# Kernel tuning notes

Hardware: AMD Instinct MI355X
Metric: run time of the kernel (lower is better)

The kernel has to match this reference:

```python
import jax, jax.numpy as jnp
import numpy as np
from jax.scipy.linalg import solve_triangular

B, L, HID, NH = 2, 1024, 1024, 4
DK = DV = 256
CONV_K, CHUNK, FIR_S_K, FIR_L_K = 4, 32, 3, 31
GATE_IN = HID + 3 * DV * 4 + DV * 4  # 5120
GATE_H = 2 * DV  # 512


def _l2norm(x):
    return x * jax.lax.rsqrt(jnp.sum(x * x, -1, keepdims=True) + 1e-6)


def _short_conv(x, w):
    # causal depthwise conv1d + silu. x: [b,l,c], w: [c,k]
    c, k = w.shape
    y = jax.lax.conv_general_dilated(x.transpose(0, 2, 1), w[:, None, :], (1,),
                                     [(k - 1, 0)], feature_group_count=c)
    return jax.nn.silu(y.transpose(0, 2, 1))


def _fir(x, f):
    # per-head depthwise causal FIR. x: [b,l,h,d], f: [h,d,k]
    b, l, h, d = x.shape
    k = f.shape[-1]
    xf = x.transpose(0, 2, 3, 1).reshape(b, h * d, l)
    y = jax.lax.conv_general_dilated(xf, f.reshape(h * d, 1, k), (1,),
                                     [(k - 1, 0)], feature_group_count=h * d)
    return y.reshape(b, h, d, l).transpose(0, 3, 1, 2)


def _delta_rule(q, k, v, beta, chunk=CHUNK):
    # q,k: [b,h,L,dk], v: [b,h,L,dv], beta: [b,h,L]; L % chunk == 0
    b, h, l, dk = q.shape
    dv = v.shape[-1]
    n = l // chunk
    q = _l2norm(q)
    k = _l2norm(k)
    v = v * beta[..., None]
    kb = k * beta[..., None]
    rs = lambda t: t.reshape(b, h, n, chunk, -1)
    q, k, v, kb = map(rs, (q, k, v, kb))
    # UT transform: serial forward substitution == unit-lower triangular solve
    A = -jnp.tril(jnp.einsum('bhncd,bhned->bhnce', kb, k), -1)  # strictly lower
    eye = jnp.eye(chunk, dtype=q.dtype)
    T = solve_triangular(eye - A, jnp.broadcast_to(eye, A.shape), lower=True)
    u = T @ v   # [b,h,n,c,dv]
    w = T @ kb  # [b,h,n,c,dk]
    mov = lambda t: jnp.moveaxis(t, 2, 0)

    def step(S, inp):
        qi, ki, ui, wi = inp  # [b,h,c,d]
        attn = jnp.tril(qi @ ki.transpose(0, 1, 3, 2))  # causal incl. diag
        u_i = ui - wi @ S
        o_i = qi @ S + attn @ u_i
        return S + ki.transpose(0, 1, 3, 2) @ u_i, o_i

    S0 = jnp.zeros((b, h, dk, dv), dtype=q.dtype)
    S, o = jax.lax.scan(step, S0, (mov(q), mov(k), mov(u), mov(w)))
    o = jnp.moveaxis(o, 0, 2).reshape(b, h, l, dv)
    return o, S


def _gate(hidden, branches, W1, b1, W2, b2, temp, eps_floor):
    def stats(p):
        m = p.mean(-1, keepdims=True)
        r = jnp.sqrt(jnp.clip((p * p).mean(-1, keepdims=True), 1e-8))
        mx = p.max(-1, keepdims=True)
        return jnp.concatenate([jnp.broadcast_to(m, p.shape),
                                jnp.broadcast_to(r, p.shape),
                                jnp.broadcast_to(mx, p.shape)], -1)

    b, l, h, d = branches[0].shape
    hb = jnp.broadcast_to(hidden[:, :, None, :], (b, l, h, hidden.shape[-1]))
    head_in = jnp.concatenate([hb] + [stats(p) for p in branches] + list(branches), -1)
    hmid = jax.nn.gelu(head_in @ W1 + b1, approximate=False)
    logits = hmid @ W2 + b2  # [b,l,h,4]
    t = jnp.clip(temp, 0.2, 10.0)[None, None, :, None]
    w = jax.nn.softmax(logits / t, -1)
    floor = jnp.clip(eps_floor, 1e-7, 0.1)[None, None]
    w = jnp.maximum(w, floor)
    return w / w.sum(-1, keepdims=True)


def setup_inputs() -> dict:
    key = jax.random.key(0)
    ks = jax.random.split(key, 16)
    s = 0.02
    inp = {
        'x': jax.random.normal(ks[0], (B, L, HID), jnp.float32),
        'Wq': jax.random.normal(ks[1], (HID, NH * DK), jnp.float32) * s,
        'Wk': jax.random.normal(ks[2], (HID, NH * DK), jnp.float32) * s,
        'Wv': jax.random.normal(ks[3], (HID, NH * DV), jnp.float32) * s,
        'Wb': jax.random.normal(ks[4], (HID, NH), jnp.float32) * s,
        'qc_w': jax.random.normal(ks[5], (NH * DK, CONV_K), jnp.float32) * 0.5,
        'kc_w': jax.random.normal(ks[6], (NH * DK, CONV_K), jnp.float32) * 0.5,
        'vc_w': jax.random.normal(ks[7], (NH * DV, CONV_K), jnp.float32) * 0.5,
        'gW1': jax.random.normal(ks[10], (GATE_IN, GATE_H), jnp.float32) * s,
        'gb1': jnp.zeros((GATE_H,), jnp.float32),
        'gW2': jax.random.normal(ks[11], (GATE_H, 4), jnp.float32) * s,
        'gb2': jnp.zeros((4,), jnp.float32),
        'temp': jnp.ones((NH,), jnp.float32),
        'eps_floor': jnp.full((NH, 4), 0.01, jnp.float32),
        'onorm_w': jnp.ones((DV,), jnp.float32),
        'Wo': jax.random.normal(ks[12], (NH * DV, HID), jnp.float32) * s,
    }
    # FIR filters: identity tap at last position + small noise (matches init intent)
    fs = jnp.zeros((NH, DV, FIR_S_K)).at[..., -1].set(1.0)
    fl = jnp.zeros((NH, DV, FIR_L_K)).at[..., -1].set(1.0)
    inp['fir_s'] = fs + s * jax.random.normal(ks[8], fs.shape, jnp.float32)
    inp['fir_l'] = fl + s * jax.random.normal(ks[9], fl.shape, jnp.float32)
    return inp


def reference(x, Wq, Wk, Wv, Wb, qc_w, kc_w, vc_w, fir_s, fir_l,
              gW1, gb1, gW2, gb2, temp, eps_floor, onorm_w, Wo):
    b, l, _ = x.shape
    q = _short_conv(x @ Wq, qc_w).reshape(b, l, NH, DK)
    k = _short_conv(x @ Wk, kc_w).reshape(b, l, NH, DK)
    v = _short_conv(x @ Wv, vc_w).reshape(b, l, NH, DV)
    beta = jax.nn.sigmoid(x @ Wb)  # [b,l,h]
    tr = lambda t: t.transpose(0, 2, 1, 3)
    delta_o, _ = _delta_rule(tr(q), tr(k), tr(v), beta.transpose(0, 2, 1))
    delta_o = tr(delta_o)  # [b,l,h,dv]
    branches = [_fir(v, fir_s), _fir(v, fir_l), delta_o, v]
    w = _gate(x, branches, gW1, gb1, gW2, gb2, temp, eps_floor)
    o = sum(w[..., i:i + 1] * branches[i] for i in range(4))
    o = o * jax.lax.rsqrt((o * o).mean(-1, keepdims=True) + 1e-5) * onorm_w
    return o.reshape(b, l, NH * DV) @ Wo
```

## Files before the change

### kernel.cpp

```cpp
#include <hip/hip_runtime.h>
#include <math.h>

#define BB 2
#define LL 1024
#define HIDD 1024
#define NH 4
#define DD 256
#define NCH 32
#define ROWS 2048
#define HROWS 8192

typedef long long i64;
typedef unsigned short u16t;
typedef unsigned int u32t;
typedef __attribute__((ext_vector_type(8))) short short8;
typedef __attribute__((ext_vector_type(4))) float f32x4;
#define MFMA_BF16(a, b, c) __builtin_amdgcn_mfma_f32_16x16x32_bf16(a, b, c, 0, 0, 0)

__device__ __forceinline__ float sigmoidf_(float x) { return 1.0f / (1.0f + expf(-x)); }

__device__ __forceinline__ u16t f2bf(float f) {
  u32t u = __float_as_uint(f);
  u = u + 0x7FFFu + ((u >> 16) & 1u);
  return (u16t)(u >> 16);
}
__device__ __forceinline__ u32t pk2(u16t a, u16t b) { return (u32t)a | ((u32t)b << 16); }

__device__ __forceinline__ u32t cvt_pk_bf16(float lo, float hi) {
  u32t r;
  asm("v_cvt_pk_bf16_f32 %0, %1, %2" : "=v"(r) : "v"(lo), "v"(hi));
  return r;
}

__device__ __forceinline__ void async_load16(const u16t* g, u16t* l) {
  __builtin_amdgcn_global_load_lds(
      (const __attribute__((address_space(1))) u32t*)g,
      (__attribute__((address_space(3))) u32t*)l, 16, 0, 0);
}

__device__ __forceinline__ void barrier_lds_only() {
  asm volatile("s_waitcnt lgkmcnt(0)" ::: "memory");
  __builtin_amdgcn_s_barrier();
  asm volatile("" ::: "memory");
}

template<int N>
__device__ __forceinline__ void block_reduce_sum(float* v, float* scratch) {
  int lane = threadIdx.x & 63, wid = threadIdx.x >> 6;
#pragma unroll
  for (int i = 0; i < N; i++) {
    float x = v[i];
#pragma unroll
    for (int off = 1; off < 64; off <<= 1) x += __shfl_xor(x, off);
    if (lane == 0) scratch[wid * N + i] = x;
  }
  __syncthreads();
#pragma unroll
  for (int i = 0; i < N; i++)
    v[i] = scratch[i] + scratch[N + i] + scratch[2 * N + i] + scratch[3 * N + i];
  __syncthreads();
}

__device__ __forceinline__ void transcast_body(
    const float* __restrict__ in, int ldin, u16t* __restrict__ out, int ldout,
    int nbi, int kbi, float (*tile)[33]) {
  int tx = threadIdx.x & 31, ty = threadIdx.x >> 5;
  int nb = nbi * 32, kb = kbi * 32;
#pragma unroll
  for (int r = 0; r < 4; r++)
    tile[ty + r * 8][tx] = in[(i64)(kb + ty + r * 8) * ldin + nb + tx];
  __syncthreads();
#pragma unroll
  for (int r = 0; r < 4; r++)
    out[(i64)(nb + ty + r * 8) * ldout + kb + tx] = f2bf(tile[tx][ty + r * 8]);
}

__global__ __launch_bounds__(256) void prep_kernel(
    const float* __restrict__ Wq, const float* __restrict__ Wk, const float* __restrict__ Wv,
    const float* __restrict__ x, const float* __restrict__ Wb,
    u16t* __restrict__ WqkvT, u16t* __restrict__ xbf, float* __restrict__ betab) {
  __shared__ float tile[32][33];
  int blk = blockIdx.x, t = threadIdx.x;
  if (blk < 3072) {
    int m = blk >> 10, bi = blk & 1023;
    const float* in = m == 0 ? Wq : m == 1 ? Wk : Wv;
    transcast_body(in, 1024, WqkvT + (i64)m * 1024 * 1024, 1024, bi & 31, bi >> 5, tile);
  } else if (blk < 5120) {
    i64 e = ((i64)(blk - 3072) * 256 + t) * 4;
    float4 v = *(const float4*)(x + e);
    uint2 o;
    o.x = pk2(f2bf(v.x), f2bf(v.y));
    o.y = pk2(f2bf(v.z), f2bf(v.w));
    *(uint2*)(xbf + e) = o;
  } else {
    int row = blk - 5120;
    float a[4] = {0, 0, 0, 0};
    for (int c = t; c < 1024; c += 256) {
      float xv = x[(i64)row * 1024 + c];
      float4 wv = *(const float4*)(Wb + c * 4);
      a[0] += xv * wv.x; a[1] += xv * wv.y; a[2] += xv * wv.z; a[3] += xv * wv.w;
    }
    block_reduce_sum<4>(a, (float*)tile);
    if (t == 0) {
#pragma unroll
      for (int g = 0; g < 4; g++) betab[row * 4 + g] = sigmoidf_(a[g]);
    }
  }
}

__device__ __forceinline__ void gemm_bt_body(
    const u16t* __restrict__ A, const u16t* __restrict__ B,
    float* __restrict__ C, int K, int ldc, int n0, int m0,
    u16t* As, u16t* Bs) {
  int t = threadIdx.x;
  int w = t >> 6, lane = t & 63;
  int l15 = lane & 15, quad = lane >> 4;
  int wm = (w & 1) * 64, wn = (w >> 1) * 64;
  f32x4 acc[4][4] = {};
  int c0 = 2 * w, c1 = 2 * w + 1;
  int srow0 = c0 * 16 + (lane >> 2);
  int srow1 = c1 * 16 + (lane >> 2);
  int scol = (lane & 3) * 8;
  const u16t* Ag0 = A + (i64)(m0 + srow0) * K + scol;
  const u16t* Ag1 = A + (i64)(m0 + srow1) * K + scol;
  const u16t* Bg0 = B + (i64)(n0 + srow0) * K + scol;
  const u16t* Bg1 = B + (i64)(n0 + srow1) * K + scol;
  u16t* As0 = As + c0 * 512;
  u16t* As1 = As + c1 * 512;
  u16t* Bs0 = Bs + c0 * 512;
  u16t* Bs1 = Bs + c1 * 512;
  for (int k0 = 0; k0 < K; k0 += 32) {
    async_load16(Ag0 + k0, As0);
    async_load16(Ag1 + k0, As1);
    async_load16(Bg0 + k0, Bs0);
    async_load16(Bg1 + k0, Bs1);
    __syncthreads();
    short8 a[4], b[4];
#pragma unroll
    for (int mt = 0; mt < 4; mt++)
      a[mt] = *(const short8*)&As[(wm + mt * 16 + l15) * 32 + quad * 8];
#pragma unroll
    for (int nt = 0; nt < 4; nt++)
      b[nt] = *(const short8*)&Bs[(wn + nt * 16 + l15) * 32 + quad * 8];
#pragma unroll
    for (int mt = 0; mt < 4; mt++)
#pragma unroll
      for (int nt = 0; nt < 4; nt++)
        acc[mt][nt] = MFMA_BF16(a[mt], b[nt], acc[mt][nt]);
    __syncthreads();
  }
#pragma unroll
  for (int mt = 0; mt < 4; mt++) {
    int r0 = m0 + wm + mt * 16 + quad * 4;
#pragma unroll
    for (int nt = 0; nt < 4; nt++) {
      int cc = n0 + wn + nt * 16 + l15;
#pragma unroll
      for (int rg = 0; rg < 4; rg++)
        C[(i64)(r0 + rg) * ldc + cc] = acc[mt][nt][rg];
    }
  }
}

__global__ __launch_bounds__(256) void gemm_bt_kernel(
    const u16t* __restrict__ A, const u16t* __restrict__ B,
    float* __restrict__ C, int K, int ldc) {
  __shared__ u16t As[128 * 32];
  __shared__ u16t Bs[128 * 32];
  gemm_bt_body(A, B, C, K, ldc, blockIdx.x * 128, blockIdx.y * 128, As, Bs);
}

__global__ __launch_bounds__(256) void conv_silu3_kernel(
    const float* __restrict__ pre, const float* __restrict__ qw,
    const float* __restrict__ kw, const float* __restrict__ vw,
    float* __restrict__ qo, float* __restrict__ ko, float* __restrict__ vo,
    u16t* __restrict__ brcat) {
  int seg = blockIdx.x >> 11;
  int row = blockIdx.x & 2047;
  int l = row & 1023;
  int c = threadIdx.x * 4;
  const float* w = seg == 0 ? qw : seg == 1 ? kw : vw;
  float* out = seg == 0 ? qo : seg == 1 ? ko : vo;
  float4 w0 = *(const float4*)(w + (i64)(c + 0) * 4);
  float4 w1 = *(const float4*)(w + (i64)(c + 1) * 4);
  float4 w2 = *(const float4*)(w + (i64)(c + 2) * 4);
  float4 w3 = *(const float4*)(w + (i64)(c + 3) * 4);
  const float* base = pre + (i64)row * 3072 + (seg << 10) + c;
  float4 x0 = *(const float4*)(base);
  float4 acc;
  acc.x = w0.w * x0.x; acc.y = w1.w * x0.y; acc.z = w2.w * x0.z; acc.w = w3.w * x0.w;
  if (l >= 1) {
    float4 xm = *(const float4*)(base - 3072);
    acc.x += w0.z * xm.x; acc.y += w1.z * xm.y; acc.z += w2.z * xm.z; acc.w += w3.z * xm.w;
  }
  if (l >= 2) {
    float4 xm = *(const float4*)(base - 2 * 3072);
    acc.x += w0.y * xm.x; acc.y += w1.y * xm.y; acc.z += w2.y * xm.z; acc.w += w3.y * xm.w;
  }
  if (l >= 3) {
    float4 xm = *(const float4*)(base - 3 * 3072);
    acc.x += w0.x * xm.x; acc.y += w1.x * xm.y; acc.z += w2.x * xm.z; acc.w += w3.x * xm.w;
  }
  float4 r;
  r.x = acc.x * sigmoidf_(acc.x);
  r.y = acc.y * sigmoidf_(acc.y);
  r.z = acc.z * sigmoidf_(acc.z);
  r.w = acc.w * sigmoidf_(acc.w);
  *(float4*)(out + (i64)row * 1024 + c) = r;
  if (seg == 2) {
    uint2 o;
    o.x = cvt_pk_bf16(r.x, r.y);
    o.y = cvt_pk_bf16(r.z, r.w);
    *(uint2*)(brcat + ((i64)row * 4 + (c >> 8)) * 1024 + 768 + (c & 255)) = o;
  }
}

__global__ __launch_bounds__(256) void preprocess_kernel(
    const float* __restrict__ q, const float* __restrict__ k, const float* __restrict__ v,
    const float* __restrict__ beta, float* __restrict__ qn, float* __restrict__ kn,
    float* __restrict__ vb, float* __restrict__ kb, u16t* __restrict__ qnbf) {
  int t = threadIdx.x, lane = t & 63, wv = t >> 6;
  int row = blockIdx.x * 4 + wv;
  i64 base = (i64)row * 256 + lane * 4;
  float4 q4 = *(const float4*)(q + base);
  float4 k4 = *(const float4*)(k + base);
  float4 v4 = *(const float4*)(v + base);
  float s2[2];
  s2[0] = q4.x * q4.x + q4.y * q4.y + q4.z * q4.z + q4.w * q4.w;
  s2[1] = k4.x * k4.x + k4.y * k4.y + k4.z * k4.z + k4.w * k4.w;
#pragma unroll
  for (int off = 1; off < 64; off <<= 1) {
    s2[0] += __shfl_xor(s2[0], off);
    s2[1] += __shfl_xor(s2[1], off);
  }
  float qi = rsqrtf(s2[0] + 1e-6f), ki = rsqrtf(s2[1] + 1e-6f);
  float bet = beta[row];
  float4 qn4, kn4, vb4, kb4;
  qn4.x = q4.x * qi; qn4.y = q4.y * qi; qn4.z = q4.z * qi; qn4.w = q4.w * qi;
  kn4.x = k4.x * ki; kn4.y = k4.y * ki; kn4.z = k4.z * ki; kn4.w = k4.w * ki;
  vb4.x = v4.x * bet; vb4.y = v4.y * bet; vb4.z = v4.z * bet; vb4.w = v4.w * bet;
  kb4.x = kn4.x * bet; kb4.y = kn4.y * bet; kb4.z = kn4.z * bet; kb4.w = kn4.w * bet;
  *(float4*)(qn + base) = qn4;
  *(float4*)(kn + base) = kn4;
  *(float4*)(vb + base) = vb4;
  *(float4*)(kb + base) = kb4;
  int b = row >> 12, l = (row >> 2) & 1023, h = row & 3;
  uint2 o;
  o.x = cvt_pk_bf16(qn4.x, qn4.y);
  o.y = cvt_pk_bf16(qn4.z, qn4.w);
  *(uint2*)(qnbf + ((i64)(b * 4 + h) * 1024 + l) * 256 + lane * 4) = o;
}

__global__ __launch_bounds__(256) void phaseA2_kernel(
    const float* __restrict__ qn, const float* __restrict__ kn,
    const float* __restrict__ vb, const float* __restrict__ kb,
    float* __restrict__ u_g, u16t* __restrict__ w_bf, u16t* __restrict__ attn_bf,
    u16t* __restrict__ knT,
    const float* __restrict__ gW1, const float* __restrict__ Wo,
    u16t* __restrict__ W1hT, u16t* __restrict__ W1bT, u16t* __restrict__ WoT,
    float* __restrict__ wsum) {
  __shared__ __attribute__((aligned(16))) char smem[37376];
  int blk = blockIdx.x, t = threadIdx.x;
  if (blk < 256) {
    float (*KN)[260] = (float(*)[260])smem;
    float (*Ms)[32] = (float(*)[32])(smem + 33280);
    int i = blk & 31, bh = blk >> 5;
    int rbase = ((bh >> 2) * LL + i * 32) * NH + (bh & 3);
    i64 bhn = blk;
#pragma unroll
    for (int ii = 0; ii < 8; ii++) {
      int fid = t + ii * 256;
      int c = fid >> 6, dq = (fid & 63) << 2;
      *(float4*)&KN[c][dq] = *(const float4*)(kn + (i64)(rbase + c * NH) * 256 + dq);
    }
    __syncthreads();
    int c = t >> 3, e0 = (t & 7) * 4;
    const float* kbp = kb + (i64)(rbase + c * NH) * 256;
    const float* qp = qn + (i64)(rbase + c * NH) * 256;
    float am[4] = {0, 0, 0, 0}, aa[4] = {0, 0, 0, 0};
    for (int d = 0; d < 256; d += 4) {
      float4 kv = *(const float4*)(kbp + d);
      float4 qv = *(const float4*)(qp + d);
#pragma unroll
      for (int z = 0; z < 4; z++) {
        float4 nv = *(const float4*)&KN[e0 + z][d];
        am[z] += kv.x * nv.x + kv.y * nv.y + kv.z * nv.z + kv.w * nv.w;
        aa[z] += qv.x * nv.x + qv.y * nv.y + qv.z * nv.z + qv.w * nv.w;
      }
    }
    {
      uint2 o;
      u16t a0 = (e0 + 0 <= c) ? f2bf(aa[0]) : 0;
      u16t a1 = (e0 + 1 <= c) ? f2bf(aa[1]) : 0;
      u16t a2 = (e0 + 2 <= c) ? f2bf(aa[2]) : 0;
      u16t a3 = (e0 + 3 <= c) ? f2bf(aa[3]) : 0;
      o.x = pk2(a0, a1); o.y = pk2(a2, a3);
      *(uint2*)(attn_bf + bhn * 1024 + c * 32 + e0) = o;
    }
#pragma unroll
    for (int z = 0; z < 4; z++) {
      int e = e0 + z;
      Ms[c][e] = (e < c) ? am[z] : 0.0f;
    }
    __syncthreads();
    float uc[32], wc[32];
#pragma unroll
    for (int cc = 0; cc < 32; cc++) {
      float uval = vb[(i64)(rbase + cc * NH) * 256 + t];
      float wval = kb[(i64)(rbase + cc * NH) * 256 + t];
#pragma unroll
      for (int c2 = 0; c2 < cc; c2++) {
        float m = Ms[cc][c2];
        uval -= m * uc[c2];
        wval -= m * wc[c2];
      }
      uc[cc] = uval; wc[cc] = wval;
      u_g[(bhn * 32 + cc) * 256 + t] = uval;
      w_bf[(bhn * 32 + cc) * 256 + t] = f2bf(-wval);
    }
    int d = t;
    u16t o[32];
#pragma unroll
    for (int cc = 0; cc < 32; cc++) o[cc] = f2bf(KN[cc][d]);
#pragma unroll
    for (int z = 0; z < 4; z++) {
      uint4 vv;
      vv.x = pk2(o[z * 8 + 0], o[z * 8 + 1]);
      vv.y = pk2(o[z * 8 + 2], o[z * 8 + 3]);
      vv.z = pk2(o[z * 8 + 4], o[z * 8 + 5]);
      vv.w = pk2(o[z * 8 + 6], o[z * 8 + 7]);
      *(uint4*)(knT + (bhn * 256 + d) * 32 + z * 8) = vv;
    }
  } else if (blk < 2304) {
    float (*tile)[33] = (float(*)[33])smem;
    int pb = blk - 256;
    if (pb < 1024) {
      int which = pb >> 9, bi = pb & 511;
      const float* in = gW1 + (which ? (i64)4096 * 512 : 0);
      transcast_body(in, 512, which ? W1bT : W1hT, 1024, bi & 15, bi >> 4, tile);
    } else {
      int bi = pb - 1024;
      transcast_body(Wo, 1024, WoT, 1024, bi & 31, bi >> 5, tile);
    }
  } else {
    int bi = blk - 2304;
    int s12 = bi >> 1, col = (bi & 1) * 256 + t;
    const float* p = gW1 + (i64)(1024 + s12 * 256) * 512 + col;
    float acc = 0.0f;
    for (int r = 0; r < 256; r++) acc += p[(i64)r * 512];
    wsum[s12 * 512 + col] = acc;
  }
}

#define SROW 264
struct ScanBuf {
  short8 m8[8];
  f32x4 uc4;
  short8 af;
  short8 kf[4];
};

__device__ void delta_scan_body(
    int blk,
    const u16t* __restrict__ wbf, const u16t* __restrict__ knT,
    const float* __restrict__ u_g, const u16t* __restrict__ qnbf,
    const u16t* __restrict__ attnbf,
    float* __restrict__ dlt, u16t* __restrict__ brcat,
    u16t* Sbf, u16t* Ubf) {
  int t = threadIdx.x, w = t >> 6, lane = t & 63;
  int l15 = lane & 15, quad = lane >> 4;
  int bh = blk & 7, jb = blk >> 3, j0 = jb * 16;
  int b_ = bh >> 2, h_ = bh & 3;
  bool isU = (w < 2);
  int wc = isU ? w : (w - 2);
  for (int idx = t; idx < 16 * SROW; idx += 256) Sbf[idx] = 0;
  f32x4 accS[4] = {};
  __syncthreads();
  __builtin_amdgcn_s_setprio(1);

  auto load_chunk = [&](int i, ScanBuf& B) {
    i64 bhn = (i64)bh * 32 + i;
    const u16t* mbase = isU
        ? wbf + (bhn * 32 + wc * 16 + l15) * 256 + quad * 8
        : qnbf + ((i64)bh * 1024 + i * 32 + wc * 16 + l15) * 256 + quad * 8;
#pragma unroll
    for (int kd = 0; kd < 8; kd++) B.m8[kd] = *(const short8*)(mbase + kd * 32);
    if (isU) {
      int cm = wc * 16 + quad * 4;
#pragma unroll
      for (int r = 0; r < 4; r++)
        B.uc4[r] = u_g[(bhn * 32 + cm + r) * 256 + j0 + l15];
    } else {
      B.af = *(const short8*)(attnbf + bhn * 1024 + (wc * 16 + l15) * 32 + quad * 8);
    }
#pragma unroll
    for (int dt = 0; dt < 4; dt++)
      B.kf[dt] = *(const short8*)(knT + (bhn * 256 + w * 64 + dt * 16 + l15) * 32 + quad * 8);
  };

  auto process = [&](int i, ScanBuf& B) {
    f32x4 zero = {};
    f32x4 ca = isU ? B.uc4 : zero;
    f32x4 cb = zero;
#pragma unroll
    for (int kd = 0; kd < 4; kd++) {
      short8 sfa = *(const short8*)&Sbf[l15 * SROW + kd * 32 + quad * 8];
      short8 sfb = *(const short8*)&Sbf[l15 * SROW + (kd + 4) * 32 + quad * 8];
      ca = MFMA_BF16(B.m8[kd], sfa, ca);
      cb = MFMA_BF16(B.m8[kd + 4], sfb, cb);
    }
    f32x4 cacc;
#pragma unroll
    for (int r = 0; r < 4; r++) cacc[r] = ca[r] + cb[r];
    if (isU) {
      int cm = wc * 16 + quad * 4;
      uint2 o;
      o.x = cvt_pk_bf16(cacc[0], cacc[1]);
      o.y = cvt_pk_bf16(cacc[2], cacc[3]);
      *(uint2*)&Ubf[l15 * 40 + cm] = o;
    }
    barrier_lds_only();
    short8 bu = *(const short8*)&Ubf[l15 * 40 + quad * 8];
    if (!isU) {
      cacc = MFMA_BF16(B.af, bu, cacc);
#pragma unroll
      for (int rg = 0; rg < 4; rg++) {
        int l = i * 32 + wc * 16 + quad * 4 + rg;
        i64 row = ((i64)b_ * 1024 + l) * 4 + h_;
        dlt[row * 256 + j0 + l15] = cacc[rg];
        brcat[row * 1024 + 512 + j0 + l15] = f2bf(cacc[rg]);
      }
    }
#pragma unroll
    for (int dt = 0; dt < 4; dt++) accS[dt] = MFMA_BF16(B.kf[dt], bu, accS[dt]);
#pragma unroll
    for (int dt = 0; dt < 4; dt++) {
      uint2 o;
      o.x = cvt_pk_bf16(accS[dt][0], accS[dt][1]);
      o.y = cvt_pk_bf16(accS[dt][2], accS[dt][3]);
      *(uint2*)&Sbf[l15 * SROW + w * 64 + dt * 16 + quad * 4] = o;
    }
    barrier_lds_only();
  };

  ScanBuf b0, b1;
  load_chunk(0, b0);
#pragma unroll 1
  for (int ii = 0; ii < 16; ii++) {
    int i = ii * 2;
    load_chunk(i + 1, b1);
    process(i, b0);
    if (ii < 15) load_chunk(i + 2, b0);
    process(i + 1, b1);
  }
  __builtin_amdgcn_s_setprio(0);
}

__device__ void fir2_body(
    int blk, const float* __restrict__ v,
    const float* __restrict__ f_s, const float* __restrict__ f_l,
    float* __restrict__ fs, float* __restrict__ fl, u16t* __restrict__ brcat) {
  int t = threadIdx.x;
  int b = blk >> 8, h = (blk >> 6) & 3, lc = blk & 63;
  int l0 = lc * 16;
  float flw[31], fsw[3];
  const float* flp = f_l + ((i64)h * 256 + t) * 31;
#pragma unroll
  for (int j = 0; j < 31; j++) flw[j] = flp[j];
  const float* fsp = f_s + ((i64)h * 256 + t) * 3;
#pragma unroll
  for (int j = 0; j < 3; j++) fsw[j] = fsp[j];
  float win[46];
#pragma unroll
  for (int r = 0; r < 46; r++) {
    int l = l0 - 30 + r;
    win[r] = (l >= 0) ? v[(((i64)b * 1024 + l) * 4 + h) * 256 + t] : 0.0f;
  }
#pragma unroll
  for (int i = 0; i < 16; i++) {
    float al = 0.0f;
#pragma unroll
    for (int j = 0; j < 31; j++) al += flw[j] * win[i + j];
    float as = fsw[0] * win[i + 28] + fsw[1] * win[i + 29] + fsw[2] * win[i + 30];
    i64 row = ((i64)b * 1024 + (l0 + i)) * 4 + h;
    fs[row * 256 + t] = as;
    fl[row * 256 + t] = al;
    brcat[row * 1024 + t] = f2bf(as);
    brcat[row * 1024 + 256 + t] = f2bf(al);
  }
}

__global__ __launch_bounds__(256) void mega5_kernel(
    const u16t* __restrict__ wbf, const u16t* __restrict__ knT,
    const float* __restrict__ u_g, const u16t* __restrict__ qnbf,
    const u16t* __restrict__ attnbf, float* __restrict__ dlt, u16t* __restrict__ brcat,
    const float* __restrict__ vbuf, const float* __restrict__ firs,
    const float* __restrict__ firl, float* __restrict__ fs, float* __restrict__ fl,
    const u16t* __restrict__ xbf, const u16t* __restrict__ W1hT,
    float* __restrict__ hbase) {
  __shared__ __attribute__((aligned(16))) char smem[16384];
  int blk = blockIdx.x;
  if (blk < 128) {
    u16t* Sbf = (u16t*)smem;
    u16t* Ubf = Sbf + 16 * SROW;
    delta_scan_body(blk, wbf, knT, u_g, qnbf, attnbf, dlt, brcat, Sbf, Ubf);
  } else if (blk < 640) {
    fir2_body(blk - 128, vbuf, firs, firl, fs, fl, brcat);
  } else {
    int bi = blk - 640;
    u16t* As = (u16t*)smem;
    u16t* Bs = As + 128 * 32;
    gemm_bt_body(xbf, W1hT, hbase, 1024, 512, (bi & 3) * 128, (bi >> 2) * 128, As, Bs);
  }
}

__global__ __launch_bounds__(256) void gatemix_kernel(
    const float* __restrict__ hbase, const float* __restrict__ brW,
    const float* __restrict__ wsum,
    const float* __restrict__ gb1, const float* __restrict__ gW2,
    const float* __restrict__ gb2, const float* __restrict__ temp,
    const float* __restrict__ epsf,
    const float* __restrict__ fs, const float* __restrict__ fl,
    const float* __restrict__ dlt, const float* __restrict__ v,
    const float* __restrict__ onw, u16t* __restrict__ out) {
  int t = threadIdx.x, lane = t & 63, wv = t >> 6;
  int row = blockIdx.x * 4 + wv;
  int bl = row >> 2, h = row & 3;
  i64 base = (i64)row * 256 + lane * 4;
  float4 vfs = *(const float4*)(fs + base);
  float4 vfl = *(const float4*)(fl + base);
  float4 vdl = *(const float4*)(dlt + base);
  float4 vvv = *(const float4*)(v + base);
  float r8[8];
  r8[0] = vfs.x + vfs.y + vfs.z + vfs.w;
  r8[1] = vfs.x * vfs.x + vfs.y * vfs.y + vfs.z * vfs.z + vfs.w * vfs.w;
  r8[2] = vfl.x + vfl.y + vfl.z + vfl.w;
  r8[3] = vfl.x * vfl.x + vfl.y * vfl.y + vfl.z * vfl.z + vfl.w * vfl.w;
  r8[4] = vdl.x + vdl.y + vdl.z + vdl.w;
  r8[5] = vdl.x * vdl.x + vdl.y * vdl.y + vdl.z * vdl.z + vdl.w * vdl.w;
  r8[6] = vvv.x + vvv.y + vvv.z + vvv.w;
  r8[7] = vvv.x * vvv.x + vvv.y * vvv.y + vvv.z * vvv.z + vvv.w * vvv.w;
#pragma unroll
  for (int off = 1; off < 64; off <<= 1) {
#pragma unroll
    for (int i = 0; i < 8; i++) r8[i] += __shfl_xor(r8[i], off);
  }
  float m4[4];
  m4[0] = fmaxf(fmaxf(vfs.x, vfs.y), fmaxf(vfs.z, vfs.w));
  m4[1] = fmaxf(fmaxf(vfl.x, vfl.y), fmaxf(vfl.z, vfl.w));
  m4[2] = fmaxf(fmaxf(vdl.x, vdl.y), fmaxf(vdl.z, vdl.w));
  m4[3] = fmaxf(fmaxf(vvv.x, vvv.y), fmaxf(vvv.z, vvv.w));
#pragma unroll
  for (int off = 1; off < 64; off <<= 1) {
#pragma unroll
    for (int i = 0; i < 4; i++) m4[i] = fmaxf(m4[i], __shfl_xor(m4[i], off));
  }
  float st[12];
#pragma unroll
  for (int p = 0; p < 4; p++) {
    st[p * 3 + 0] = r8[p * 2] * (1.0f / 256.0f);
    st[p * 3 + 1] = sqrtf(fmaxf(r8[p * 2 + 1] * (1.0f / 256.0f), 1e-8f));
    st[p * 3 + 2] = m4[p];
  }
  float lg[4] = {0, 0, 0, 0};
#pragma unroll
  for (int jj = 0; jj < 8; jj++) {
    int o = jj * 64 + lane;
    float hm = hbase[(i64)bl * 512 + o] + brW[(i64)row * 512 + o] + gb1[o];
#pragma unroll
    for (int s = 0; s < 12; s++) hm += st[s] * wsum[s * 512 + o];
    float ge = 0.5f * hm * (1.0f + erff(hm * 0.70710678118654752f));
    float4 w2 = *(const float4*)(gW2 + o * 4);
    lg[0] += ge * w2.x; lg[1] += ge * w2.y; lg[2] += ge * w2.z; lg[3] += ge * w2.w;
  }
#pragma unroll
  for (int off = 1; off < 64; off <<= 1) {
#pragma unroll
    for (int i = 0; i < 4; i++) lg[i] += __shfl_xor(lg[i], off);
  }
  float tt = fminf(fmaxf(temp[h], 0.2f), 10.0f);
  float l0 = (lg[0] + gb2[0]) / tt;
  float l1 = (lg[1] + gb2[1]) / tt;
  float l2 = (lg[2] + gb2[2]) / tt;
  float l3 = (lg[3] + gb2[3]) / tt;
  float m = fmaxf(fmaxf(l0, l1), fmaxf(l2, l3));
  float e0 = expf(l0 - m), e1 = expf(l1 - m), e2 = expf(l2 - m), e3 = expf(l3 - m);
  float ssum = e0 + e1 + e2 + e3;
  float w0 = e0 / ssum, w1 = e1 / ssum, w2 = e2 / ssum, w3 = e3 / ssum;
  w0 = fmaxf(w0, fminf(fmaxf(epsf[h * 4 + 0], 1e-7f), 0.1f));
  w1 = fmaxf(w1, fminf(fmaxf(epsf[h * 4 + 1], 1e-7f), 0.1f));
  w2 = fmaxf(w2, fminf(fmaxf(epsf[h * 4 + 2], 1e-7f), 0.1f));
  w3 = fmaxf(w3, fminf(fmaxf(epsf[h * 4 + 3], 1e-7f), 0.1f));
  float s2 = w0 + w1 + w2 + w3;
  float g0 = w0 / s2, g1 = w1 / s2, g2 = w2 / s2, g3 = w3 / s2;
  float4 o4;
  o4.x = g0 * vfs.x + g1 * vfl.x + g2 * vdl.x + g3 * vvv.x;
  o4.y = g0 * vfs.y + g1 * vfl.y + g2 * vdl.y + g3 * vvv.y;
  o4.z = g0 * vfs.z + g1 * vfl.z + g2 * vdl.z + g3 * vvv.z;
  o4.w = g0 * vfs.w + g1 * vfl.w + g2 * vdl.w + g3 * vvv.w;
  float ss = o4.x * o4.x + o4.y * o4.y + o4.z * o4.z + o4.w * o4.w;
#pragma unroll
  for (int off = 1; off < 64; off <<= 1) ss += __shfl_xor(ss, off);
  float scale = rsqrtf(ss * (1.0f / 256.0f) + 1e-5f);
  float4 ow4 = *(const float4*)(onw + lane * 4);
  uint2 ow;
  ow.x = cvt_pk_bf16(o4.x * scale * ow4.x, o4.y * scale * ow4.y);
  ow.y = cvt_pk_bf16(o4.z * scale * ow4.z, o4.w * scale * ow4.w);
  *(uint2*)(out + (i64)bl * 1024 + h * 256 + lane * 4) = ow;
}

extern "C" void kernel_launch(void* const* d_in, const int* in_sizes, int n_in,
                              void* d_out, int out_size, void* d_ws, size_t ws_size,
                              hipStream_t stream) {
  (void)in_sizes; (void)n_in; (void)out_size; (void)ws_size;
  const float* x    = (const float*)d_in[0];
  const float* Wq   = (const float*)d_in[1];
  const float* Wk   = (const float*)d_in[2];
  const float* Wv   = (const float*)d_in[3];
  const float* Wb   = (const float*)d_in[4];
  const float* qcw  = (const float*)d_in[5];
  const float* kcw  = (const float*)d_in[6];
  const float* vcw  = (const float*)d_in[7];
  const float* gW1  = (const float*)d_in[8];
  const float* gb1  = (const float*)d_in[9];
  const float* gW2  = (const float*)d_in[10];
  const float* gb2  = (const float*)d_in[11];
  const float* temp = (const float*)d_in[12];
  const float* epsf = (const float*)d_in[13];
  const float* onw  = (const float*)d_in[14];
  const float* Wo   = (const float*)d_in[15];
  const float* firs = (const float*)d_in[16];
  const float* firl = (const float*)d_in[17];
  float* out = (float*)d_out;

  float* ws = (float*)d_ws;
  float* qkv_pre  = ws + 0;
  float* branchW  = ws + 0;
  float* hbase    = ws + 4194304;
  u16t*  W1hT     = (u16t*)(ws + 5242880);
  u16t*  W1bT     = (u16t*)(ws + 5505024);
  u16t*  WoT      = (u16t*)(ws + 5767168);
  u16t*  brcat    = (u16t*)(ws + 6291456);
  float* qbuf     = ws + 10485760; float* qn = qbuf;
  float* kbuf     = ws + 12582912; float* kn = kbuf;
  float* vbuf     = ws + 14680064;
  float* vb       = ws + 16777216;
  u16t*  omix_bf  = (u16t*)(ws + 16777216);
  float* kb       = ws + 18874368;
  float* dlt      = ws + 18874368;
  float* u_g      = ws + 20971520;
  u16t*  w_bf     = (u16t*)(ws + 23068672);
  u16t*  qn_bf    = (u16t*)(ws + 24117248);
  u16t*  knT      = (u16t*)(ws + 25165824);
  u16t*  attn_bf  = (u16t*)(ws + 26214400);
  float* fs       = ws + 26345472;
  float* fl       = ws + 28442624;
  u16t*  xbf      = (u16t*)(ws + 30539776);
  u16t*  WqkvT    = (u16t*)(ws + 31588352);
  float* betab    = ws + 33161216;
  float* wsum     = ws + 33267712;

  prep_kernel<<<7168, 256, 0, stream>>>(Wq, Wk, Wv, x, Wb, WqkvT, xbf, betab);
  gemm_bt_kernel<<<dim3(24, 16), 256, 0, stream>>>(xbf, WqkvT, qkv_pre, 1024, 3072);
  conv_silu3_kernel<<<6144, 256, 0, stream>>>(qkv_pre, qcw, kcw, vcw, qbuf, kbuf, vbuf, brcat);
  preprocess_kernel<<<2048, 256, 0, stream>>>(qbuf, kbuf, vbuf, betab, qn, kn, vb, kb, qn_bf);
  phaseA2_kernel<<<2328, 256, 0, stream>>>(qn, kn, vb, kb, u_g, w_bf, attn_bf, knT,
                                           gW1, Wo, W1hT, W1bT, WoT, wsum);
  mega5_kernel<<<704, 256, 0, stream>>>(w_bf, knT, u_g, qn_bf, attn_bf, dlt, brcat,
                                        vbuf, firs, firl, fs, fl,
                                        xbf, W1hT, hbase);
  gemm_bt_kernel<<<dim3(4, 64), 256, 0, stream>>>(brcat, W1bT, branchW, 1024, 512);
  gatemix_kernel<<<2048, 256, 0, stream>>>(hbase, branchW, wsum, gb1, gW2, gb2,
                                           temp, epsf, fs, fl, dlt, vbuf, onw, omix_bf);
  gemm_bt_kernel<<<dim3(8, 16), 256, 0, stream>>>(omix_bf, WoT, out, 1024, 1024);
}
```

Before: 328.0 us.

## Double-buffer LDS tiles in the bf16 GEMM body to overlap loads with MFMA

```diff
diff --git a/kernel.cpp b/kernel.cpp
--- a/kernel.cpp
+++ b/kernel.cpp
@@ -125,39 +125,46 @@
   const u16t* Ag1 = A + (i64)(m0 + srow1) * K + scol;
   const u16t* Bg0 = B + (i64)(n0 + srow0) * K + scol;
   const u16t* Bg1 = B + (i64)(n0 + srow1) * K + scol;
-  u16t* As0 = As + c0 * 512;
-  u16t* As1 = As + c1 * 512;
-  u16t* Bs0 = Bs + c0 * 512;
-  u16t* Bs1 = Bs + c1 * 512;
-  for (int k0 = 0; k0 < K; k0 += 32) {
-    async_load16(Ag0 + k0, As0);
-    async_load16(Ag1 + k0, As1);
-    async_load16(Bg0 + k0, Bs0);
-    async_load16(Bg1 + k0, Bs1);
-    __syncthreads();
+  int lb0 = c0 * 512, lb1 = c1 * 512;
+  async_load16(Ag0, As + lb0);
+  async_load16(Ag1, As + lb1);
+  async_load16(Bg0, Bs + lb0);
+  async_load16(Bg1, Bs + lb1);
+  __syncthreads();
+  int nt = K >> 5;
+  for (int ti = 0; ti < nt; ++ti) {
+    int cur = (ti & 1) << 12;
+    if (ti + 1 < nt) {
+      int nxt = ((ti + 1) & 1) << 12;
+      int k = (ti + 1) << 5;
+      async_load16(Ag0 + k, As + nxt + lb0);
+      async_load16(Ag1 + k, As + nxt + lb1);
+      async_load16(Bg0 + k, Bs + nxt + lb0);
+      async_load16(Bg1 + k, Bs + nxt + lb1);
+    }
     short8 a[4], b[4];
 #pragma unroll
     for (int mt = 0; mt < 4; mt++)
-      a[mt] = *(const short8*)&As[(wm + mt * 16 + l15) * 32 + quad * 8];
-#pragma unroll
-    for (int nt = 0; nt < 4; nt++)
-      b[nt] = *(const short8*)&Bs[(wn + nt * 16 + l15) * 32 + quad * 8];
+      a[mt] = *(const short8*)&As[cur + (wm + mt * 16 + l15) * 32 + quad * 8];
+#pragma unroll
+    for (int ntt = 0; ntt < 4; ntt++)
+      b[ntt] = *(const short8*)&Bs[cur + (wn + ntt * 16 + l15) * 32 + quad * 8];
 #pragma unroll
     for (int mt = 0; mt < 4; mt++)
 #pragma unroll
-      for (int nt = 0; nt < 4; nt++)
-        acc[mt][nt] = MFMA_BF16(a[mt], b[nt], acc[mt][nt]);
+      for (int ntt = 0; ntt < 4; ntt++)
+        acc[mt][ntt] = MFMA_BF16(a[mt], b[ntt], acc[mt][ntt]);
     __syncthreads();
   }
 #pragma unroll
   for (int mt = 0; mt < 4; mt++) {
     int r0 = m0 + wm + mt * 16 + quad * 4;
 #pragma unroll
-    for (int nt = 0; nt < 4; nt++) {
-      int cc = n0 + wn + nt * 16 + l15;
+    for (int nt2 = 0; nt2 < 4; nt2++) {
+      int cc = n0 + wn + nt2 * 16 + l15;
 #pragma unroll
       for (int rg = 0; rg < 4; rg++)
-        C[(i64)(r0 + rg) * ldc + cc] = acc[mt][nt][rg];
+        C[(i64)(r0 + rg) * ldc + cc] = acc[mt][nt2][rg];
     }
   }
 }
@@ -165,8 +172,8 @@
 __global__ __launch_bounds__(256) void gemm_bt_kernel(
     const u16t* __restrict__ A, const u16t* __restrict__ B,
     float* __restrict__ C, int K, int ldc) {
-  __shared__ u16t As[128 * 32];
-  __shared__ u16t Bs[128 * 32];
+  __shared__ u16t As[2 * 128 * 32];
+  __shared__ u16t Bs[2 * 128 * 32];
   gemm_bt_body(A, B, C, K, ldc, blockIdx.x * 128, blockIdx.y * 128, As, Bs);
 }
 
@@ -498,7 +505,7 @@
     const float* __restrict__ firl, float* __restrict__ fs, float* __restrict__ fl,
     const u16t* __restrict__ xbf, const u16t* __restrict__ W1hT,
     float* __restrict__ hbase) {
-  __shared__ __attribute__((aligned(16))) char smem[16384];
+  __shared__ __attribute__((aligned(16))) char smem[32768];
   int blk = blockIdx.x;
   if (blk < 128) {
     u16t* Sbf = (u16t*)smem;
@@ -509,7 +516,7 @@
   } else {
     int bi = blk - 640;
     u16t* As = (u16t*)smem;
-    u16t* Bs = As + 128 * 32;
+    u16t* Bs = As + 2 * 128 * 32;
     gemm_bt_body(xbf, W1hT, hbase, 1024, 512, (bi & 3) * 128, (bi >> 2) * 128, As, Bs);
   }
 }
```

Result: faster. 316.6 us (-3.5%).
